# Kernel tuning notes

Measured on AMD Instinct MI355X. Metric: run time of the kernel, lower is better.

## Reference

```python
import jax, jax.numpy as jnp
import numpy as np


def setup_inputs() -> dict:
    key = jax.random.key(0)
    k1, k2, k3, k4, k5, k6 = jax.random.split(key, 6)
    B, N, T, F = 16, 256, 64, 128  # batch, num_hnodes==in_dim==out_dim, time_win, feat
    x = jax.random.normal(k1, (B, N, T, F), dtype=jnp.float32)
    entryid = jax.random.randint(k2, (B, N, T), 0, N, dtype=jnp.int64)
    jobid = jax.random.randint(k3, (B, N, T), 0, 8, dtype=jnp.int64)
    rackid = jax.random.randint(k4, (B, N, T), 0, 16, dtype=jnp.int64)
    full_weight = jax.random.normal(k5, (N, N), dtype=jnp.float32) * 0.05
    bias = jax.random.normal(k6, (N,), dtype=jnp.float32) * 0.01
    gamma = jnp.ones((N,), dtype=jnp.float32)
    beta = jnp.zeros((N,), dtype=jnp.float32)
    return {"x": x, "entryid": entryid, "jobid": jobid, "rackid": rackid,
            "full_weight": full_weight, "bias": bias, "gamma": gamma, "beta": beta}


def reference(x, entryid, jobid, rackid, full_weight, bias, gamma, beta):
    # NOTE: in the original torch module the LayerNorm output is overwritten
    # (y = x.permute(...)) and MaskLinear never adds its bias; we reproduce
    # that exact math, so norm/bias are dead w.r.t. the output.
    B, N, T, F = x.shape  # N == in_dim == out_dim == num_hnodes, T == time_win
    out_features = full_weight.shape[0]

    inp = jnp.transpose(x, (0, 2, 3, 1))  # [B, T, F, N]

    # gather per-(batch,node,time) weight columns: [out, B, N, T]
    weight = full_weight[:, entryid.reshape(-1)].reshape(out_features, B, N, T)

    # job-equality mask: [B, N, N, T] -> permuted to [N, B, N, T]
    same_job = (jobid[:, :, None, :] == jobid[:, None, :, :]) \
               & (jobid[:, :, None, :] != 0) & (jobid[:, None, :, :] != 0)
    mask = jnp.transpose(same_job, (1, 0, 2, 3)).astype(x.dtype)

    masked_weight = weight * mask  # [out(=N), B, N, T] via broadcast over dim0

    # einsum 'bijk,lbki->bijl' with i=T, j=F, k=N, l=out
    y = jnp.einsum('bijk,lbki->bijl', inp, masked_weight)
    y = jax.nn.relu(y)            # dropout is identity at eval
    y = jnp.transpose(y, (0, 3, 1, 2))  # [B, out, T, F]
    return x + y
```

## Files before the change

### kernel.cpp

```cpp
#include <hip/hip_runtime.h>
#include <stdint.h>

typedef float  f32x4 __attribute__((ext_vector_type(4)));
typedef short  s16x8 __attribute__((ext_vector_type(8)));
typedef short  s16x4 __attribute__((ext_vector_type(4)));
typedef unsigned int uint32;

#define B_ 16
#define N_ 256
#define T_ 64
#define F_ 128
#define KT 32
#define NT 8

#define SUBT 512
#define X_TILE_STR (16 * SUBT)
#define X_OFF 0
#define W_OFF (NT * X_TILE_STR)
#define LDS_SZ (W_OFF + 32 * SUBT)

#define TRREAD(dst, addr) \
  asm volatile("ds_read_b64_tr_b16 %0, %1" : "=v"(dst) : "v"(addr))

#define LGKM_FENCE() asm volatile("s_waitcnt lgkmcnt(0)" ::: "memory")
#define BAR()                                    \
  do {                                           \
    LGKM_FENCE();                                \
    __builtin_amdgcn_s_barrier();                \
    asm volatile("" ::: "memory");               \
  } while (0)

__device__ __forceinline__ unsigned short f2bf(float f) {
  union { float f; unsigned int u; } v; v.f = f;
  unsigned int u = v.u;
  return (unsigned short)((u + 0x7fffu + ((u >> 16) & 1u)) >> 16);
}
__device__ __forceinline__ float bf2f(unsigned short h) {
  union { unsigned int u; float f; } v; v.u = ((unsigned int)h) << 16;
  return v.f;
}

__global__ void wtrans_kernel(const float* __restrict__ fw,
                              unsigned short* __restrict__ fwTb) {
  int c = blockIdx.x;
  int l = threadIdx.x;
  fwTb[c * N_ + l] = f2bf(fw[l * N_ + c]);
}

__global__ __launch_bounds__(512, 2) void fused_kernel(
    const float* __restrict__ x,
    const int* __restrict__ entry,
    const int* __restrict__ job,
    const unsigned short* __restrict__ fwTb,
    float* __restrict__ out) {
  __shared__ __align__(16) char smem[LDS_SZ];
  const uint32 lds_u = (uint32)(uintptr_t)(&smem[0]);

  const int tid = threadIdx.x;
  const int bid = blockIdx.x;
  const int b = bid >> 6;
  const int t = bid & 63;

  const int wk  = tid & 31;
  const int wlg = tid >> 5;

  int er[8], jr[8], jlr[16];
#pragma unroll
  for (int i = 0; i < 8; ++i) {
    er[i] = entry[(b * N_ + i * KT + wk) * T_ + t];
    jr[i] = job[(b * N_ + i * KT + wk) * T_ + t];
  }
#pragma unroll
  for (int i = 0; i < 16; ++i)
    jlr[i] = job[(b * N_ + wlg * 16 + i) * T_ + t];

  const int xk  = tid >> 4;
  const int xf0 = (tid & 15) << 3;
  const float* xsrc = x + ((b * N_ + xk) * T_ + t) * F_ + xf0;
#define XLD(i)                                                            \
  f32x4 q##i##a = *(const f32x4*)(xsrc + (i) * (KT * T_ * F_));           \
  f32x4 q##i##b = *(const f32x4*)(xsrc + (i) * (KT * T_ * F_) + 4);
  XLD(0) XLD(1) XLD(2) XLD(3) XLD(4) XLD(5) XLD(6) XLD(7)
#undef XLD

  uint32 ep0 = 0, ep1 = 0, jp0 = 0, jp1 = 0;
#pragma unroll
  for (int i = 0; i < 4; ++i) {
    ep0 |= ((uint32)(er[i] & 255)) << (8 * i);
    ep1 |= ((uint32)(er[i + 4] & 255)) << (8 * i);
    jp0 |= ((uint32)(jr[i] & 255)) << (8 * i);
    jp1 |= ((uint32)(jr[i + 4] & 255)) << (8 * i);
  }
  uint64_t jl80 = 0, jl81 = 0;
#pragma unroll
  for (int i = 0; i < 8; ++i) {
    jl80 |= ((uint64_t)(jlr[i] & 255)) << (8 * i);
    jl81 |= ((uint64_t)(jlr[i + 8] & 255)) << (8 * i);
  }

  const uint32 wwr_base =
      (uint32)(((wk >> 4) * 16 + wlg) * SUBT + (wk & 15) * 32);
  {
    const int ev = (int)(ep0 & 255);
    const unsigned char gjk = (unsigned char)(jp0 & 255);
    const unsigned short* wrow = fwTb + ev * N_ + wlg * 16;
    s16x8 gv0 = *(const s16x8*)(wrow);
    s16x8 gv1 = *(const s16x8*)(wrow + 8);
    s16x8 m0, m1;
#pragma unroll
    for (int i = 0; i < 8; ++i) {
      const unsigned char a0 = (unsigned char)(jl80 >> (8 * i));
      const unsigned char a1 = (unsigned char)(jl81 >> (8 * i));
      m0[i] = (gjk != 0 && a0 == gjk) ? gv0[i] : (short)0;
      m1[i] = (gjk != 0 && a1 == gjk) ? gv1[i] : (short)0;
    }
    *(s16x8*)(smem + W_OFF + wwr_base) = m0;
    *(s16x8*)(smem + W_OFF + wwr_base + 16) = m1;
  }

  const uint32 xdst_in = (uint32)((((xk >> 4) * 8 + (xf0 >> 4)) * SUBT) +
                                  ((xk & 15) * 32) + ((xf0 & 15) * 2));
#define XST(i)                                                            \
  {                                                                       \
    s16x8 pk;                                                             \
    _Pragma("unroll") for (int _j = 0; _j < 4; ++_j) {                    \
      pk[_j]     = (short)f2bf(q##i##a[_j]);                              \
      pk[_j + 4] = (short)f2bf(q##i##b[_j]);                              \
    }                                                                     \
    *(s16x8*)(smem + X_OFF + (i) * X_TILE_STR + xdst_in) = pk;            \
  }
  XST(0) XST(1) XST(2) XST(3) XST(4) XST(5) XST(6) XST(7)
#undef XST
  BAR();

  const int lane = tid & 63;
  const int wid  = tid >> 6;
  const int wl   = wid & 3;
  const int wf   = wid >> 2;

  f32x4 acc[4][4];
#pragma unroll
  for (int i = 0; i < 4; ++i)
#pragma unroll
    for (int j = 0; j < 4; ++j) acc[i][j] = (f32x4){0.f, 0.f, 0.f, 0.f};

  for (int kt = 0; kt < NT; ++kt) {
    s16x8 pv0, pv1;
    unsigned char pjk = 0;
    if (kt + 1 < NT) {
      const uint32 esel = (kt + 1 < 4) ? ep0 : ep1;
      const uint32 jsel = (kt + 1 < 4) ? jp0 : jp1;
      const int sh = ((kt + 1) & 3) * 8;
      const int ev = (int)((esel >> sh) & 255);
      pjk = (unsigned char)((jsel >> sh) & 255);
      const unsigned short* wrow = fwTb + ev * N_ + wlg * 16;
      pv0 = *(const s16x8*)(wrow);
      pv1 = *(const s16x8*)(wrow + 8);
    }

    s16x4 ah[4][2], bh[4][2];
    {
      const uint32 wbase = lds_u + W_OFF + (uint32)(lane * 8);
      const uint32 xbase =
          lds_u + X_OFF + (uint32)(kt * X_TILE_STR) + (uint32)(lane * 8);
#pragma unroll
      for (int li = 0; li < 4; ++li) {
        TRREAD(ah[li][0], wbase + (uint32)((wl * 4 + li) * SUBT));
        TRREAD(ah[li][1], wbase + (uint32)((16 + wl * 4 + li) * SUBT));
      }
#pragma unroll
      for (int fi = 0; fi < 4; ++fi) {
        TRREAD(bh[fi][0], xbase + (uint32)((wf * 4 + fi) * SUBT));
        TRREAD(bh[fi][1], xbase + (uint32)((8 + wf * 4 + fi) * SUBT));
      }
      LGKM_FENCE();
      __builtin_amdgcn_sched_barrier(0);
    }
    if (kt + 1 < NT) BAR();

#pragma unroll
    for (int li = 0; li < 4; ++li) {
      s16x8 af = __builtin_shufflevector(ah[li][0], ah[li][1],
                                         0, 1, 2, 3, 4, 5, 6, 7);
#pragma unroll
      for (int fi = 0; fi < 4; ++fi) {
        s16x8 bf = __builtin_shufflevector(bh[fi][0], bh[fi][1],
                                           0, 1, 2, 3, 4, 5, 6, 7);
        acc[li][fi] =
            __builtin_amdgcn_mfma_f32_16x16x32_bf16(af, bf, acc[li][fi], 0, 0, 0);
      }
    }
    __builtin_amdgcn_sched_barrier(0);

    if (kt + 1 < NT) {
      s16x8 m0, m1;
#pragma unroll
      for (int i = 0; i < 8; ++i) {
        const unsigned char a0 = (unsigned char)(jl80 >> (8 * i));
        const unsigned char a1 = (unsigned char)(jl81 >> (8 * i));
        m0[i] = (pjk != 0 && a0 == pjk) ? pv0[i] : (short)0;
        m1[i] = (pjk != 0 && a1 == pjk) ? pv1[i] : (short)0;
      }
      *(s16x8*)(smem + W_OFF + wwr_base) = m0;
      *(s16x8*)(smem + W_OFF + wwr_base + 16) = m1;
      BAR();
    }
  }

  const int g4   = (lane >> 4) * 4;
  const int fcol = lane & 15;
#pragma unroll
  for (int li = 0; li < 4; ++li) {
    const int Lb = wl * 4 + li;
    const uint32 rb = lds_u + X_OFF + (uint32)((Lb >> 1) * X_TILE_STR +
                       ((Lb & 1) * 8) * SUBT + lane * 8);
    s16x4 xr[4];
#pragma unroll
    for (int fi = 0; fi < 4; ++fi) {
      TRREAD(xr[fi], rb + (uint32)((wf * 4 + fi) * SUBT));
    }
    LGKM_FENCE();
    __builtin_amdgcn_sched_barrier(0);
    const int l0 = Lb * 16 + g4;
#pragma unroll
    for (int fi = 0; fi < 4; ++fi) {
      const int f = (wf * 4 + fi) * 16 + fcol;
      float* op = out + ((b * N_ + l0) * T_ + t) * F_ + f;
#pragma unroll
      for (int r = 0; r < 4; ++r) {
        float y = acc[li][fi][r];
        y = y > 0.f ? y : 0.f;
        op[r * (T_ * F_)] = bf2f((unsigned short)xr[fi][r]) + y;
      }
    }
  }
}

extern "C" void kernel_launch(void* const* d_in, const int* in_sizes, int n_in,
                              void* d_out, int out_size, void* d_ws,
                              size_t ws_size, hipStream_t stream) {
  (void)in_sizes; (void)n_in; (void)out_size; (void)ws_size;
  const float* x     = (const float*)d_in[0];
  const int*   entry = (const int*)d_in[1];
  const int*   job   = (const int*)d_in[2];
  const float* fw    = (const float*)d_in[4];
  unsigned short* fwTb = (unsigned short*)d_ws;

  hipLaunchKernelGGL(wtrans_kernel, dim3(N_), dim3(N_), 0, stream, fw, fwTb);
  hipLaunchKernelGGL(fused_kernel, dim3(B_ * T_), dim3(512), 0, stream,
                     x, entry, job, (const unsigned short*)fwTb, (float*)d_out);
}
```

Baseline: 81.69 us.

## Double-buffer x tiles in LDS and re-read fp32 x for the residual

Replaces the full 8-tile bf16 x staging in LDS with a two-buffer scheme. Each next x chunk is loaded from global memory during the current MFMA step and stored after it, which shrinks LDS use and may allow more blocks per CU. The residual add now re-reads x in fp32 from global memory instead of using the bf16 copy in LDS, fixing precision at the cost of extra global reads. The prefetch also adds global-load latency to each loop iteration.

New measurement: 92.55 us. 13.3% more time.

```diff
diff --git a/kernel.cpp b/kernel.cpp
--- a/kernel.cpp
+++ b/kernel.cpp
@@ -14,9 +14,9 @@
 #define NT 8
 
 #define SUBT 512
-#define X_TILE_STR (16 * SUBT)
+#define X_BUF_STR (16 * SUBT)
 #define X_OFF 0
-#define W_OFF (NT * X_TILE_STR)
+#define W_OFF (2 * X_BUF_STR)
 #define LDS_SZ (W_OFF + 32 * SUBT)
 
 #define TRREAD(dst, addr) \
@@ -34,10 +34,6 @@
   union { float f; unsigned int u; } v; v.f = f;
   unsigned int u = v.u;
   return (unsigned short)((u + 0x7fffu + ((u >> 16) & 1u)) >> 16);
-}
-__device__ __forceinline__ float bf2f(unsigned short h) {
-  union { unsigned int u; float f; } v; v.u = ((unsigned int)h) << 16;
-  return v.f;
 }
 
 __global__ void wtrans_kernel(const float* __restrict__ fw,
@@ -77,11 +73,8 @@
   const int xk  = tid >> 4;
   const int xf0 = (tid & 15) << 3;
   const float* xsrc = x + ((b * N_ + xk) * T_ + t) * F_ + xf0;
-#define XLD(i)                                                            \
-  f32x4 q##i##a = *(const f32x4*)(xsrc + (i) * (KT * T_ * F_));           \
-  f32x4 q##i##b = *(const f32x4*)(xsrc + (i) * (KT * T_ * F_) + 4);
-  XLD(0) XLD(1) XLD(2) XLD(3) XLD(4) XLD(5) XLD(6) XLD(7)
-#undef XLD
+  f32x4 c0a = *(const f32x4*)(xsrc);
+  f32x4 c0b = *(const f32x4*)(xsrc + 4);
 
   uint32 ep0 = 0, ep1 = 0, jp0 = 0, jp1 = 0;
 #pragma unroll
@@ -120,17 +113,15 @@
 
   const uint32 xdst_in = (uint32)((((xk >> 4) * 8 + (xf0 >> 4)) * SUBT) +
                                   ((xk & 15) * 32) + ((xf0 & 15) * 2));
-#define XST(i)                                                            \
-  {                                                                       \
-    s16x8 pk;                                                             \
-    _Pragma("unroll") for (int _j = 0; _j < 4; ++_j) {                    \
-      pk[_j]     = (short)f2bf(q##i##a[_j]);                              \
-      pk[_j + 4] = (short)f2bf(q##i##b[_j]);                              \
-    }                                                                     \
-    *(s16x8*)(smem + X_OFF + (i) * X_TILE_STR + xdst_in) = pk;            \
-  }
-  XST(0) XST(1) XST(2) XST(3) XST(4) XST(5) XST(6) XST(7)
-#undef XST
+  {
+    s16x8 pk;
+#pragma unroll
+    for (int j = 0; j < 4; ++j) {
+      pk[j]     = (short)f2bf(c0a[j]);
+      pk[j + 4] = (short)f2bf(c0b[j]);
+    }
+    *(s16x8*)(smem + X_OFF + xdst_in) = pk;
+  }
   BAR();
 
   const int lane = tid & 63;
@@ -145,6 +136,14 @@
     for (int j = 0; j < 4; ++j) acc[i][j] = (f32x4){0.f, 0.f, 0.f, 0.f};
 
   for (int kt = 0; kt < NT; ++kt) {
+    f32x4 p0, p1;
+    if (kt + 1 < NT) {
+      const float* src =
+          x + ((b * N_ + (kt + 1) * KT + xk) * T_ + t) * F_ + xf0;
+      p0 = *(const f32x4*)(src);
+      p1 = *(const f32x4*)(src + 4);
+    }
+
     s16x8 pv0, pv1;
     unsigned char pjk = 0;
     if (kt + 1 < NT) {
@@ -162,7 +161,7 @@
     {
       const uint32 wbase = lds_u + W_OFF + (uint32)(lane * 8);
       const uint32 xbase =
-          lds_u + X_OFF + (uint32)(kt * X_TILE_STR) + (uint32)(lane * 8);
+          lds_u + X_OFF + (uint32)((kt & 1) * X_BUF_STR) + (uint32)(lane * 8);
 #pragma unroll
       for (int li = 0; li < 4; ++li) {
         TRREAD(ah[li][0], wbase + (uint32)((wl * 4 + li) * SUBT));
@@ -203,6 +202,14 @@
       }
       *(s16x8*)(smem + W_OFF + wwr_base) = m0;
       *(s16x8*)(smem + W_OFF + wwr_base + 16) = m1;
+
+      s16x8 pk;
+#pragma unroll
+      for (int j = 0; j < 4; ++j) {
+        pk[j]     = (short)f2bf(p0[j]);
+        pk[j + 4] = (short)f2bf(p1[j]);
+      }
+      *(s16x8*)(smem + X_OFF + ((kt + 1) & 1) * X_BUF_STR + xdst_in) = pk;
       BAR();
     }
   }
@@ -211,26 +218,17 @@
   const int fcol = lane & 15;
 #pragma unroll
   for (int li = 0; li < 4; ++li) {
-    const int Lb = wl * 4 + li;
-    const uint32 rb = lds_u + X_OFF + (uint32)((Lb >> 1) * X_TILE_STR +
-                       ((Lb & 1) * 8) * SUBT + lane * 8);
-    s16x4 xr[4];
-#pragma unroll
-    for (int fi = 0; fi < 4; ++fi) {
-      TRREAD(xr[fi], rb + (uint32)((wf * 4 + fi) * SUBT));
-    }
-    LGKM_FENCE();
-    __builtin_amdgcn_sched_barrier(0);
-    const int l0 = Lb * 16 + g4;
+    const int l0 = (wl * 4 + li) * 16 + g4;
 #pragma unroll
     for (int fi = 0; fi < 4; ++fi) {
       const int f = (wf * 4 + fi) * 16 + fcol;
+      const float* xp = x + ((b * N_ + l0) * T_ + t) * F_ + f;
       float* op = out + ((b * N_ + l0) * T_ + t) * F_ + f;
 #pragma unroll
       for (int r = 0; r < 4; ++r) {
         float y = acc[li][fi][r];
         y = y > 0.f ? y : 0.f;
-        op[r * (T_ * F_)] = bf2f((unsigned short)xr[fi][r]) + y;
+        op[r * (T_ * F_)] = xp[r * (T_ * F_)] + y;
       }
     }
   }
```

## Split F dimension across two 256-thread blocks per (batch,time)

Applied to the files above, without the earlier changes.

Each (b,t) tile is now handled by two blocks, each covering half of the feature dimension, with 256 threads instead of 512. The X tile in LDS is halved, so more blocks can be resident and the grid doubles, which is meant to improve occupancy and load balance across CUs. In exchange, each block rebuilds the full masked weight tile, so the gather, mask computation and job-id loads are duplicated across the two halves.

New measurement: 90.27 us. 10.5% more time.

```diff
diff --git a/kernel.cpp b/kernel.cpp
--- a/kernel.cpp
+++ b/kernel.cpp
@@ -12,9 +12,10 @@
 #define F_ 128
 #define KT 32
 #define NT 8
+#define NF 64
 
 #define SUBT 512
-#define X_TILE_STR (16 * SUBT)
+#define X_TILE_STR (8 * SUBT)
 #define X_OFF 0
 #define W_OFF (NT * X_TILE_STR)
 #define LDS_SZ (W_OFF + 32 * SUBT)
@@ -47,7 +48,7 @@
   fwTb[c * N_ + l] = f2bf(fw[l * N_ + c]);
 }
 
-__global__ __launch_bounds__(512, 2) void fused_kernel(
+__global__ __launch_bounds__(256, 2) void fused_kernel(
     const float* __restrict__ x,
     const int* __restrict__ entry,
     const int* __restrict__ job,
@@ -58,25 +59,28 @@
 
   const int tid = threadIdx.x;
   const int bid = blockIdx.x;
-  const int b = bid >> 6;
-  const int t = bid & 63;
+  const int b  = bid >> 7;
+  const int t  = (bid >> 1) & 63;
+  const int fh = bid & 1;
 
   const int wk  = tid & 31;
   const int wlg = tid >> 5;
 
-  int er[8], jr[8], jlr[16];
+  int er[8], jr[8], jlrA[16], jlrB[16];
 #pragma unroll
   for (int i = 0; i < 8; ++i) {
     er[i] = entry[(b * N_ + i * KT + wk) * T_ + t];
     jr[i] = job[(b * N_ + i * KT + wk) * T_ + t];
   }
 #pragma unroll
-  for (int i = 0; i < 16; ++i)
-    jlr[i] = job[(b * N_ + wlg * 16 + i) * T_ + t];
-
-  const int xk  = tid >> 4;
-  const int xf0 = (tid & 15) << 3;
-  const float* xsrc = x + ((b * N_ + xk) * T_ + t) * F_ + xf0;
+  for (int i = 0; i < 16; ++i) {
+    jlrA[i] = job[(b * N_ + wlg * 16 + i) * T_ + t];
+    jlrB[i] = job[(b * N_ + (wlg + 8) * 16 + i) * T_ + t];
+  }
+
+  const int xk  = tid >> 3;
+  const int xf0 = (tid & 7) << 3;
+  const float* xsrc = x + ((b * N_ + xk) * T_ + t) * F_ + fh * NF + xf0;
 #define XLD(i)                                                            \
   f32x4 q##i##a = *(const f32x4*)(xsrc + (i) * (KT * T_ * F_));           \
   f32x4 q##i##b = *(const f32x4*)(xsrc + (i) * (KT * T_ * F_) + 4);
@@ -91,34 +95,46 @@
     jp0 |= ((uint32)(jr[i] & 255)) << (8 * i);
     jp1 |= ((uint32)(jr[i + 4] & 255)) << (8 * i);
   }
-  uint64_t jl80 = 0, jl81 = 0;
+  uint64_t jlA0 = 0, jlA1 = 0, jlB0 = 0, jlB1 = 0;
 #pragma unroll
   for (int i = 0; i < 8; ++i) {
-    jl80 |= ((uint64_t)(jlr[i] & 255)) << (8 * i);
-    jl81 |= ((uint64_t)(jlr[i + 8] & 255)) << (8 * i);
-  }
-
-  const uint32 wwr_base =
+    jlA0 |= ((uint64_t)(jlrA[i] & 255)) << (8 * i);
+    jlA1 |= ((uint64_t)(jlrA[i + 8] & 255)) << (8 * i);
+    jlB0 |= ((uint64_t)(jlrB[i] & 255)) << (8 * i);
+    jlB1 |= ((uint64_t)(jlrB[i + 8] & 255)) << (8 * i);
+  }
+
+  const uint32 wwrA =
       (uint32)(((wk >> 4) * 16 + wlg) * SUBT + (wk & 15) * 32);
+  const uint32 wwrB =
+      (uint32)(((wk >> 4) * 16 + wlg + 8) * SUBT + (wk & 15) * 32);
   {
     const int ev = (int)(ep0 & 255);
     const unsigned char gjk = (unsigned char)(jp0 & 255);
-    const unsigned short* wrow = fwTb + ev * N_ + wlg * 16;
-    s16x8 gv0 = *(const s16x8*)(wrow);
-    s16x8 gv1 = *(const s16x8*)(wrow + 8);
-    s16x8 m0, m1;
+    const unsigned short* wrow = fwTb + ev * N_;
+    s16x8 gA0 = *(const s16x8*)(wrow + wlg * 16);
+    s16x8 gA1 = *(const s16x8*)(wrow + wlg * 16 + 8);
+    s16x8 gB0 = *(const s16x8*)(wrow + (wlg + 8) * 16);
+    s16x8 gB1 = *(const s16x8*)(wrow + (wlg + 8) * 16 + 8);
+    s16x8 mA0, mA1, mB0, mB1;
 #pragma unroll
     for (int i = 0; i < 8; ++i) {
-      const unsigned char a0 = (unsigned char)(jl80 >> (8 * i));
-      const unsigned char a1 = (unsigned char)(jl81 >> (8 * i));
-      m0[i] = (gjk != 0 && a0 == gjk) ? gv0[i] : (short)0;
-      m1[i] = (gjk != 0 && a1 == gjk) ? gv1[i] : (short)0;
-    }
-    *(s16x8*)(smem + W_OFF + wwr_base) = m0;
-    *(s16x8*)(smem + W_OFF + wwr_base + 16) = m1;
-  }
-
-  const uint32 xdst_in = (uint32)((((xk >> 4) * 8 + (xf0 >> 4)) * SUBT) +
+      const unsigned char a0 = (unsigned char)(jlA0 >> (8 * i));
+      const unsigned char a1 = (unsigned char)(jlA1 >> (8 * i));
+      const unsigned char b0 = (unsigned char)(jlB0 >> (8 * i));
+      const unsigned char b1 = (unsigned char)(jlB1 >> (8 * i));
+      mA0[i] = (gjk != 0 && a0 == gjk) ? gA0[i] : (short)0;
+      mA1[i] = (gjk != 0 && a1 == gjk) ? gA1[i] : (short)0;
+      mB0[i] = (gjk != 0 && b0 == gjk) ? gB0[i] : (short)0;
+      mB1[i] = (gjk != 0 && b1 == gjk) ? gB1[i] : (short)0;
+    }
+    *(s16x8*)(smem + W_OFF + wwrA) = mA0;
+    *(s16x8*)(smem + W_OFF + wwrA + 16) = mA1;
+    *(s16x8*)(smem + W_OFF + wwrB) = mB0;
+    *(s16x8*)(smem + W_OFF + wwrB + 16) = mB1;
+  }
+
+  const uint32 xdst_in = (uint32)((((xk >> 4) * 4 + (xf0 >> 4)) * SUBT) +
                                   ((xk & 15) * 32) + ((xf0 & 15) * 2));
 #define XST(i)                                                            \
   {                                                                       \
@@ -134,9 +150,7 @@
   BAR();
 
   const int lane = tid & 63;
-  const int wid  = tid >> 6;
-  const int wl   = wid & 3;
-  const int wf   = wid >> 2;
+  const int wl   = tid >> 6;
 
   f32x4 acc[4][4];
 #pragma unroll
@@ -145,7 +159,7 @@
     for (int j = 0; j < 4; ++j) acc[i][j] = (f32x4){0.f, 0.f, 0.f, 0.f};
 
   for (int kt = 0; kt < NT; ++kt) {
-    s16x8 pv0, pv1;
+    s16x8 pA0, pA1, pB0, pB1;
     unsigned char pjk = 0;
     if (kt + 1 < NT) {
       const uint32 esel = (kt + 1 < 4) ? ep0 : ep1;
@@ -153,9 +167,11 @@
       const int sh = ((kt + 1) & 3) * 8;
       const int ev = (int)((esel >> sh) & 255);
       pjk = (unsigned char)((jsel >> sh) & 255);
-      const unsigned short* wrow = fwTb + ev * N_ + wlg * 16;
-      pv0 = *(const s16x8*)(wrow);
-      pv1 = *(const s16x8*)(wrow + 8);
+      const unsigned short* wrow = fwTb + ev * N_;
+      pA0 = *(const s16x8*)(wrow + wlg * 16);
+      pA1 = *(const s16x8*)(wrow + wlg * 16 + 8);
+      pB0 = *(const s16x8*)(wrow + (wlg + 8) * 16);
+      pB1 = *(const s16x8*)(wrow + (wlg + 8) * 16 + 8);
     }
 
     s16x4 ah[4][2], bh[4][2];
@@ -170,8 +186,8 @@
       }
 #pragma unroll
       for (int fi = 0; fi < 4; ++fi) {
-        TRREAD(bh[fi][0], xbase + (uint32)((wf * 4 + fi) * SUBT));
-        TRREAD(bh[fi][1], xbase + (uint32)((8 + wf * 4 + fi) * SUBT));
+        TRREAD(bh[fi][0], xbase + (uint32)(fi * SUBT));
+        TRREAD(bh[fi][1], xbase + (uint32)((4 + fi) * SUBT));
       }
       LGKM_FENCE();
       __builtin_amdgcn_sched_barrier(0);
@@ -193,16 +209,22 @@
     __builtin_amdgcn_sched_barrier(0);
 
     if (kt + 1 < NT) {
-      s16x8 m0, m1;
+      s16x8 mA0, mA1, mB0, mB1;
 #pragma unroll
       for (int i = 0; i < 8; ++i) {
-        const unsigned char a0 = (unsigned char)(jl80 >> (8 * i));
-        const unsigned char a1 = (unsigned char)(jl81 >> (8 * i));
-        m0[i] = (pjk != 0 && a0 == pjk) ? pv0[i] : (short)0;
-        m1[i] = (pjk != 0 && a1 == pjk) ? pv1[i] : (short)0;
-      }
-      *(s16x8*)(smem + W_OFF + wwr_base) = m0;
-      *(s16x8*)(smem + W_OFF + wwr_base + 16) = m1;
+        const unsigned char a0 = (unsigned char)(jlA0 >> (8 * i));
+        const unsigned char a1 = (unsigned char)(jlA1 >> (8 * i));
+        const unsigned char b0 = (unsigned char)(jlB0 >> (8 * i));
+        const unsigned char b1 = (unsigned char)(jlB1 >> (8 * i));
+        mA0[i] = (pjk != 0 && a0 == pjk) ? pA0[i] : (short)0;
+        mA1[i] = (pjk != 0 && a1 == pjk) ? pA1[i] : (short)0;
+        mB0[i] = (pjk != 0 && b0 == pjk) ? pB0[i] : (short)0;
+        mB1[i] = (pjk != 0 && b1 == pjk) ? pB1[i] : (short)0;
+      }
+      *(s16x8*)(smem + W_OFF + wwrA) = mA0;
+      *(s16x8*)(smem + W_OFF + wwrA + 16) = mA1;
+      *(s16x8*)(smem + W_OFF + wwrB) = mB0;
+      *(s16x8*)(smem + W_OFF + wwrB + 16) = mB1;
       BAR();
     }
   }
@@ -213,18 +235,18 @@
   for (int li = 0; li < 4; ++li) {
     const int Lb = wl * 4 + li;
     const uint32 rb = lds_u + X_OFF + (uint32)((Lb >> 1) * X_TILE_STR +
-                       ((Lb & 1) * 8) * SUBT + lane * 8);
+                       ((Lb & 1) * 4) * SUBT + lane * 8);
     s16x4 xr[4];
 #pragma unroll
     for (int fi = 0; fi < 4; ++fi) {
-      TRREAD(xr[fi], rb + (uint32)((wf * 4 + fi) * SUBT));
+      TRREAD(xr[fi], rb + (uint32)(fi * SUBT));
     }
     LGKM_FENCE();
     __builtin_amdgcn_sched_barrier(0);
     const int l0 = Lb * 16 + g4;
 #pragma unroll
     for (int fi = 0; fi < 4; ++fi) {
-      const int f = (wf * 4 + fi) * 16 + fcol;
+      const int f = fh * NF + fi * 16 + fcol;
       float* op = out + ((b * N_ + l0) * T_ + t) * F_ + f;
 #pragma unroll
       for (int r = 0; r < 4; ++r) {
@@ -247,6 +269,6 @@
   unsigned short* fwTb = (unsigned short*)d_ws;
 
   hipLaunchKernelGGL(wtrans_kernel, dim3(N_), dim3(N_), 0, stream, fw, fwTb);
-  hipLaunchKernelGGL(fused_kernel, dim3(B_ * T_), dim3(512), 0, stream,
+  hipLaunchKernelGGL(fused_kernel, dim3(B_ * T_ * 2), dim3(256), 0, stream,
                      x, entry, job, (const unsigned short*)fwTb, (float*)d_out);
 }
```

## Make blocks persistent over four tiles with double-buffered X prefetch

Applied to the files above, without the earlier changes.

Each block now processes four consecutive (batch,time) tiles instead of one. While computing the current tile, it loads the next tile's x slices, entry and job ids into registers, then writes the bf16-converted x into a second LDS buffer. The goal is to hide global load latency behind MFMA work and to amortise the per-block setup. In exchange, LDS usage nearly doubles and the grid shrinks to a quarter, which may reduce occupancy and the number of CUs kept busy.

Measured after the change: 89.08 us. 1.09x slower.

```diff
diff --git a/kernel.cpp b/kernel.cpp
--- a/kernel.cpp
+++ b/kernel.cpp
@@ -12,11 +12,13 @@
 #define F_ 128
 #define KT 32
 #define NT 8
+#define NTILES 4
 
 #define SUBT 512
 #define X_TILE_STR (16 * SUBT)
+#define X_BUFSZ (NT * X_TILE_STR)
 #define X_OFF 0
-#define W_OFF (NT * X_TILE_STR)
+#define W_OFF (2 * X_BUFSZ)
 #define LDS_SZ (W_OFF + 32 * SUBT)
 
 #define TRREAD(dst, addr) \
@@ -57,12 +59,18 @@
   const uint32 lds_u = (uint32)(uintptr_t)(&smem[0]);
 
   const int tid = threadIdx.x;
-  const int bid = blockIdx.x;
-  const int b = bid >> 6;
-  const int t = bid & 63;
+  int tile = blockIdx.x * NTILES;
+  int b = tile >> 6;
+  int t = tile & 63;
 
   const int wk  = tid & 31;
   const int wlg = tid >> 5;
+  const int xk  = tid >> 4;
+  const int xf0 = (tid & 15) << 3;
+  const uint32 xdst_in = (uint32)((((xk >> 4) * 8 + (xf0 >> 4)) * SUBT) +
+                                  ((xk & 15) * 32) + ((xf0 & 15) * 2));
+  const uint32 wwr_base =
+      (uint32)(((wk >> 4) * 16 + wlg) * SUBT + (wk & 15) * 32);
 
   int er[8], jr[8], jlr[16];
 #pragma unroll
@@ -74,8 +82,6 @@
   for (int i = 0; i < 16; ++i)
     jlr[i] = job[(b * N_ + wlg * 16 + i) * T_ + t];
 
-  const int xk  = tid >> 4;
-  const int xf0 = (tid & 15) << 3;
   const float* xsrc = x + ((b * N_ + xk) * T_ + t) * F_ + xf0;
 #define XLD(i)                                                            \
   f32x4 q##i##a = *(const f32x4*)(xsrc + (i) * (KT * T_ * F_));           \
@@ -98,8 +104,6 @@
     jl81 |= ((uint64_t)(jlr[i + 8] & 255)) << (8 * i);
   }
 
-  const uint32 wwr_base =
-      (uint32)(((wk >> 4) * 16 + wlg) * SUBT + (wk & 15) * 32);
   {
     const int ev = (int)(ep0 & 255);
     const unsigned char gjk = (unsigned char)(jp0 & 255);
@@ -118,8 +122,6 @@
     *(s16x8*)(smem + W_OFF + wwr_base + 16) = m1;
   }
 
-  const uint32 xdst_in = (uint32)((((xk >> 4) * 8 + (xf0 >> 4)) * SUBT) +
-                                  ((xk & 15) * 32) + ((xf0 & 15) * 2));
 #define XST(i)                                                            \
   {                                                                       \
     s16x8 pk;                                                             \
@@ -138,100 +140,187 @@
   const int wl   = wid & 3;
   const int wf   = wid >> 2;
 
-  f32x4 acc[4][4];
-#pragma unroll
-  for (int i = 0; i < 4; ++i)
-#pragma unroll
-    for (int j = 0; j < 4; ++j) acc[i][j] = (f32x4){0.f, 0.f, 0.f, 0.f};
-
-  for (int kt = 0; kt < NT; ++kt) {
-    s16x8 pv0, pv1;
-    unsigned char pjk = 0;
-    if (kt + 1 < NT) {
-      const uint32 esel = (kt + 1 < 4) ? ep0 : ep1;
-      const uint32 jsel = (kt + 1 < 4) ? jp0 : jp1;
-      const int sh = ((kt + 1) & 3) * 8;
-      const int ev = (int)((esel >> sh) & 255);
-      pjk = (unsigned char)((jsel >> sh) & 255);
-      const unsigned short* wrow = fwTb + ev * N_ + wlg * 16;
-      pv0 = *(const s16x8*)(wrow);
-      pv1 = *(const s16x8*)(wrow + 8);
-    }
-
-    s16x4 ah[4][2], bh[4][2];
-    {
-      const uint32 wbase = lds_u + W_OFF + (uint32)(lane * 8);
-      const uint32 xbase =
-          lds_u + X_OFF + (uint32)(kt * X_TILE_STR) + (uint32)(lane * 8);
+  uint32 nep0 = 0, nep1 = 0, njp0 = 0, njp1 = 0;
+  uint64_t njl0 = 0, njl1 = 0;
+
+  for (int g = 0; g < NTILES; ++g) {
+    const uint32 xcur = (uint32)((g & 1) * X_BUFSZ);
+    const uint32 xnxt = (uint32)(((g & 1) ^ 1) * X_BUFSZ);
+    const bool pf = (g + 1 < NTILES);
+    const int ntile = pf ? tile + 1 : tile;
+    const int nb = ntile >> 6, ntt = ntile & 63;
+
+    f32x4 acc[4][4];
+#pragma unroll
+    for (int i = 0; i < 4; ++i)
+#pragma unroll
+      for (int j = 0; j < 4; ++j) acc[i][j] = (f32x4){0.f, 0.f, 0.f, 0.f};
+
+    f32x4 pvA, pvB;
+    f32x4 cvA, cvB;
+
+    for (int kt = 0; kt < NT; ++kt) {
+      const bool has_next = (kt < NT - 1) || pf;
+
+      s16x8 wv0, wv1;
+      unsigned char wjk = 0;
+      uint64_t mj0 = 0, mj1 = 0;
+      if (has_next) {
+        int ev;
+        if (kt < NT - 1) {
+          const uint32 esel = (kt + 1 < 4) ? ep0 : ep1;
+          const uint32 jsel = (kt + 1 < 4) ? jp0 : jp1;
+          const int sh = ((kt + 1) & 3) * 8;
+          ev = (int)((esel >> sh) & 255);
+          wjk = (unsigned char)((jsel >> sh) & 255);
+          mj0 = jl80; mj1 = jl81;
+        } else {
+          ev = (int)(nep0 & 255);
+          wjk = (unsigned char)(njp0 & 255);
+          mj0 = njl0; mj1 = njl1;
+        }
+        const unsigned short* wrow = fwTb + ev * N_ + wlg * 16;
+        wv0 = *(const s16x8*)(wrow);
+        wv1 = *(const s16x8*)(wrow + 8);
+      }
+
+      if (pf && kt == 4) {
+        int e2[8], j2[8], l2[16];
+#pragma unroll
+        for (int i = 0; i < 8; ++i) {
+          e2[i] = entry[(nb * N_ + i * KT + wk) * T_ + ntt];
+          j2[i] = job[(nb * N_ + i * KT + wk) * T_ + ntt];
+        }
+#pragma unroll
+        for (int i = 0; i < 16; ++i)
+          l2[i] = job[(nb * N_ + wlg * 16 + i) * T_ + ntt];
+        nep0 = nep1 = njp0 = njp1 = 0; njl0 = njl1 = 0;
+#pragma unroll
+        for (int i = 0; i < 4; ++i) {
+          nep0 |= ((uint32)(e2[i] & 255)) << (8 * i);
+          nep1 |= ((uint32)(e2[i + 4] & 255)) << (8 * i);
+          njp0 |= ((uint32)(j2[i] & 255)) << (8 * i);
+          njp1 |= ((uint32)(j2[i + 4] & 255)) << (8 * i);
+        }
+#pragma unroll
+        for (int i = 0; i < 8; ++i) {
+          njl0 |= ((uint64_t)(l2[i] & 255)) << (8 * i);
+          njl1 |= ((uint64_t)(l2[i + 8] & 255)) << (8 * i);
+        }
+      }
+
+      if (pf) {
+        const float* src =
+            x + ((nb * N_ + kt * KT + xk) * T_ + ntt) * F_ + xf0;
+        cvA = *(const f32x4*)(src);
+        cvB = *(const f32x4*)(src + 4);
+      }
+
+      s16x4 ah[4][2], bh[4][2];
+      {
+        const uint32 wbase = lds_u + W_OFF + (uint32)(lane * 8);
+        const uint32 xbase = lds_u + X_OFF + xcur +
+                             (uint32)(kt * X_TILE_STR) + (uint32)(lane * 8);
+#pragma unroll
+        for (int li = 0; li < 4; ++li) {
+          TRREAD(ah[li][0], wbase + (uint32)((wl * 4 + li) * SUBT));
+          TRREAD(ah[li][1], wbase + (uint32)((16 + wl * 4 + li) * SUBT));
+        }
+#pragma unroll
+        for (int fi = 0; fi < 4; ++fi) {
+          TRREAD(bh[fi][0], xbase + (uint32)((wf * 4 + fi) * SUBT));
+          TRREAD(bh[fi][1], xbase + (uint32)((8 + wf * 4 + fi) * SUBT));
+        }
+        LGKM_FENCE();
+        __builtin_amdgcn_sched_barrier(0);
+      }
+      if (has_next) BAR();
+
 #pragma unroll
       for (int li = 0; li < 4; ++li) {
-        TRREAD(ah[li][0], wbase + (uint32)((wl * 4 + li) * SUBT));
-        TRREAD(ah[li][1], wbase + (uint32)((16 + wl * 4 + li) * SUBT));
-      }
+        s16x8 af = __builtin_shufflevector(ah[li][0], ah[li][1],
+                                           0, 1, 2, 3, 4, 5, 6, 7);
+#pragma unroll
+        for (int fi = 0; fi < 4; ++fi) {
+          s16x8 bf = __builtin_shufflevector(bh[fi][0], bh[fi][1],
+                                             0, 1, 2, 3, 4, 5, 6, 7);
+          acc[li][fi] = __builtin_amdgcn_mfma_f32_16x16x32_bf16(
+              af, bf, acc[li][fi], 0, 0, 0);
+        }
+      }
+      __builtin_amdgcn_sched_barrier(0);
+
+      if (pf && kt >= 1) {
+        s16x8 pk;
+#pragma unroll
+        for (int j = 0; j < 4; ++j) {
+          pk[j]     = (short)f2bf(pvA[j]);
+          pk[j + 4] = (short)f2bf(pvB[j]);
+        }
+        *(s16x8*)(smem + X_OFF + xnxt + (uint32)((kt - 1) * X_TILE_STR) +
+                  xdst_in) = pk;
+      }
+      if (pf) { pvA = cvA; pvB = cvB; }
+
+      if (has_next) {
+        s16x8 m0, m1;
+#pragma unroll
+        for (int i = 0; i < 8; ++i) {
+          const unsigned char a0 = (unsigned char)(mj0 >> (8 * i));
+          const unsigned char a1 = (unsigned char)(mj1 >> (8 * i));
+          m0[i] = (wjk != 0 && a0 == wjk) ? wv0[i] : (short)0;
+          m1[i] = (wjk != 0 && a1 == wjk) ? wv1[i] : (short)0;
+        }
+        *(s16x8*)(smem + W_OFF + wwr_base) = m0;
+        *(s16x8*)(smem + W_OFF + wwr_base + 16) = m1;
+        BAR();
+      }
+    }
+
+    if (pf) {
+      s16x8 pk;
+#pragma unroll
+      for (int j = 0; j < 4; ++j) {
+        pk[j]     = (short)f2bf(pvA[j]);
+        pk[j + 4] = (short)f2bf(pvB[j]);
+      }
+      *(s16x8*)(smem + X_OFF + xnxt + (uint32)(7 * X_TILE_STR) + xdst_in) = pk;
+    }
+
+    const int g4   = (lane >> 4) * 4;
+    const int fcol = lane & 15;
+#pragma unroll
+    for (int li = 0; li < 4; ++li) {
+      const int Lb = wl * 4 + li;
+      const uint32 rb = lds_u + X_OFF + xcur +
+                        (uint32)((Lb >> 1) * X_TILE_STR +
+                                 ((Lb & 1) * 8) * SUBT + lane * 8);
+      s16x4 xr[4];
 #pragma unroll
       for (int fi = 0; fi < 4; ++fi) {
-        TRREAD(bh[fi][0], xbase + (uint32)((wf * 4 + fi) * SUBT));
-        TRREAD(bh[fi][1], xbase + (uint32)((8 + wf * 4 + fi) * SUBT));
+        TRREAD(xr[fi], rb + (uint32)((wf * 4 + fi) * SUBT));
       }
       LGKM_FENCE();
       __builtin_amdgcn_sched_barrier(0);
-    }
-    if (kt + 1 < NT) BAR();
-
-#pragma unroll
-    for (int li = 0; li < 4; ++li) {
-      s16x8 af = __builtin_shufflevector(ah[li][0], ah[li][1],
-                                         0, 1, 2, 3, 4, 5, 6, 7);
+      const int l0 = Lb * 16 + g4;
 #pragma unroll
       for (int fi = 0; fi < 4; ++fi) {
-        s16x8 bf = __builtin_shufflevector(bh[fi][0], bh[fi][1],
-                                           0, 1, 2, 3, 4, 5, 6, 7);
-        acc[li][fi] =
-            __builtin_amdgcn_mfma_f32_16x16x32_bf16(af, bf, acc[li][fi], 0, 0, 0);
-      }
-    }
-    __builtin_amdgcn_sched_barrier(0);
-
-    if (kt + 1 < NT) {
-      s16x8 m0, m1;
-#pragma unroll
-      for (int i = 0; i < 8; ++i) {
-        const unsigned char a0 = (unsigned char)(jl80 >> (8 * i));
-        const unsigned char a1 = (unsigned char)(jl81 >> (8 * i));
-        m0[i] = (pjk != 0 && a0 == pjk) ? pv0[i] : (short)0;
-        m1[i] = (pjk != 0 && a1 == pjk) ? pv1[i] : (short)0;
-      }
-      *(s16x8*)(smem + W_OFF + wwr_base) = m0;
-      *(s16x8*)(smem + W_OFF + wwr_base + 16) = m1;
+        const int f = (wf * 4 + fi) * 16 + fcol;
+        float* op = out + ((b * N_ + l0) * T_ + t) * F_ + f;
+#pragma unroll
+        for (int r = 0; r < 4; ++r) {
+          float y = acc[li][fi][r];
+          y = y > 0.f ? y : 0.f;
+          op[r * (T_ * F_)] = bf2f((unsigned short)xr[fi][r]) + y;
+        }
+      }
+    }
+
+    if (pf) {
       BAR();
-    }
-  }
-
-  const int g4   = (lane >> 4) * 4;
-  const int fcol = lane & 15;
-#pragma unroll
-  for (int li = 0; li < 4; ++li) {
-    const int Lb = wl * 4 + li;
-    const uint32 rb = lds_u + X_OFF + (uint32)((Lb >> 1) * X_TILE_STR +
-                       ((Lb & 1) * 8) * SUBT + lane * 8);
-    s16x4 xr[4];
-#pragma unroll
-    for (int fi = 0; fi < 4; ++fi) {
-      TRREAD(xr[fi], rb + (uint32)((wf * 4 + fi) * SUBT));
-    }
-    LGKM_FENCE();
-    __builtin_amdgcn_sched_barrier(0);
-    const int l0 = Lb * 16 + g4;
-#pragma unroll
-    for (int fi = 0; fi < 4; ++fi) {
-      const int f = (wf * 4 + fi) * 16 + fcol;
-      float* op = out + ((b * N_ + l0) * T_ + t) * F_ + f;
-#pragma unroll
-      for (int r = 0; r < 4; ++r) {
-        float y = acc[li][fi][r];
-        y = y > 0.f ? y : 0.f;
-        op[r * (T_ * F_)] = bf2f((unsigned short)xr[fi][r]) + y;
-      }
+      ep0 = nep0; ep1 = nep1; jp0 = njp0; jp1 = njp1;
+      jl80 = njl0; jl81 = njl1;
+      tile = ntile; b = nb; t = ntt;
     }
   }
 }
@@ -247,6 +336,7 @@
   unsigned short* fwTb = (unsigned short*)d_ws;
 
   hipLaunchKernelGGL(wtrans_kernel, dim3(N_), dim3(N_), 0, stream, fw, fwTb);
-  hipLaunchKernelGGL(fused_kernel, dim3(B_ * T_), dim3(512), 0, stream,
-                     x, entry, job, (const unsigned short*)fwTb, (float*)d_out);
-}
+  hipLaunchKernelGGL(fused_kernel, dim3((B_ * T_) / NTILES), dim3(512), 0,
+                     stream, x, entry, job, (const unsigned short*)fwTb,
+                     (float*)d_out);
+}
```
